# Kernel tuning notes

Measured on AMD Instinct MI355X. Metric: run time of the kernel, lower is better.

## Reference

```python
import jax, jax.numpy as jnp
import numpy as np

N = 50000        # n_nodes
E = 640000       # n_edges
D = 128          # d_model (in_dim == out_dim)
H = 8            # num_heads
DH = D // H      # head dim = 16
EPS = 1e-5


def _batchnorm(x, g, b):
    # BatchNorm1d, training-mode batch statistics (biased variance)
    mu = jnp.mean(x, axis=0)
    var = jnp.mean((x - mu) ** 2, axis=0)
    return (x - mu) * jax.lax.rsqrt(var + EPS) * g + b


def setup_inputs() -> dict:
    key = jax.random.key(0)
    ks = jax.random.split(key, 16)
    s = 0.05
    h = jax.random.normal(ks[0], (N, D), jnp.float32)
    src = jax.random.randint(ks[1], (E,), 0, N)
    # guarantee every node has >= 1 incoming edge (avoids z == 0)
    dst = jnp.concatenate([jnp.arange(N), jax.random.randint(ks[2], (E - N,), 0, N)])
    return {
        "h": h,
        "src": src,
        "dst": dst,
        "WQ": jax.random.normal(ks[3], (D, D), jnp.float32) * s,
        "WK": jax.random.normal(ks[4], (D, D), jnp.float32) * s,
        "WV": jax.random.normal(ks[5], (D, D), jnp.float32) * s,
        "WO": jax.random.normal(ks[6], (D, D), jnp.float32) * s,
        "bO": jnp.zeros((D,), jnp.float32),
        "W1": jax.random.normal(ks[7], (2 * D, D), jnp.float32) * s,
        "b1": jnp.zeros((2 * D,), jnp.float32),
        "W2": jax.random.normal(ks[8], (D, 2 * D), jnp.float32) * s,
        "b2": jnp.zeros((D,), jnp.float32),
        "bn1_g": jnp.ones((D,), jnp.float32),
        "bn1_b": jnp.zeros((D,), jnp.float32),
        "bn2_g": jnp.ones((D,), jnp.float32),
        "bn2_b": jnp.zeros((D,), jnp.float32),
    }


def reference(h, src, dst, WQ, WK, WV, WO, bO, W1, b1, W2, b2, bn1_g, bn1_b, bn2_g, bn2_b):
    n = h.shape[0]
    # projections -> [N, H, DH]
    Q = (h @ WQ.T).reshape(n, H, DH)
    K = (h @ WK.T).reshape(n, H, DH)
    V = (h @ WV.T).reshape(n, H, DH)
    # per-edge score: sum(K[src] * Q[dst]) -> [E, H]; clamp/exp (scaled_exp)
    score = jnp.sum(K[src] * Q[dst], axis=-1) / np.sqrt(DH)
    score = jnp.exp(jnp.clip(score, -5.0, 5.0))
    # scatter-sum weighted values and normalizers to destination nodes
    wV = jax.ops.segment_sum(V[src] * score[..., None], dst, num_segments=n)  # [N,H,DH]
    z = jax.ops.segment_sum(score, dst, num_segments=n)                       # [N,H]
    attn = (wV / z[..., None]).reshape(n, D)
    # O projection + residual + BN1
    h1 = _batchnorm(h + (attn @ WO.T + bO), bn1_g, bn1_b)
    # FFN + residual + BN2
    f = jax.nn.relu(h1 @ W1.T + b1) @ W2.T + b2
    return _batchnorm(h1 + f, bn2_g, bn2_b)
```

## Files before the change

### kernel.cpp

```cpp
#include <hip/hip_runtime.h>
#include <math.h>


#define ND128 16384
typedef _Float16 f16;
typedef __attribute__((ext_vector_type(8))) _Float16 h8;
typedef __attribute__((ext_vector_type(4))) _Float16 h4;
typedef __attribute__((ext_vector_type(2))) _Float16 h2;
typedef __attribute__((ext_vector_type(4))) float f4;

__device__ __forceinline__ float fdot2h(h2 a, h2 b) {
#if __has_builtin(__builtin_amdgcn_fdot2)
    return __builtin_amdgcn_fdot2(a, b, 0.f, false);
#else
    return (float)a[0] * (float)b[0] + (float)a[1] * (float)b[1];
#endif
}

__device__ __forceinline__ float fast_exp2(float x) {
#if __has_builtin(__builtin_amdgcn_exp2f)
    return __builtin_amdgcn_exp2f(x);
#else
    return exp2f(x);
#endif
}

template <int CTRL>
__device__ __forceinline__ float dppadd(float x) {
    int t = __builtin_amdgcn_update_dpp(0, __float_as_int(x), CTRL, 0xF, 0xF, false);
    return x + __int_as_float(t);
}
__device__ __forceinline__ float wsum8(float p) {
    p = dppadd<0xB1>(p);
    p = dppadd<0x4E>(p);
    p = dppadd<0x141>(p);
    return p;
}

__global__ __launch_bounds__(256) void k_prep(
    const float* __restrict__ h, f16* __restrict__ hb,
    const float* __restrict__ WQ, const float* __restrict__ WK,
    const float* __restrict__ WV, const float* __restrict__ WO,
    const float* __restrict__ W2,
    f16* __restrict__ Wqb, f16* __restrict__ Wkb,
    f16* __restrict__ Wvb, f16* __restrict__ Wob, f16* __restrict__ W2b,
    float* __restrict__ bn, int* __restrict__ cursor, int N)
{
    const int slab = blockIdx.x, my = blockIdx.y;
    const int tid = threadIdx.x;
    if (my == 0) {
        if (tid < 128) {
            int ci = slab * 128 + tid;
            if (ci < N) cursor[ci] = 0;
        }
        if (slab == 6) { bn[tid] = 0.f; bn[tid + 256] = 0.f; }
    }
#pragma unroll
    for (int it2 = 0; it2 < 4; ++it2) {
        int it = my * 4 + it2;
        int cid = it * 256 + tid;
        int lane = cid & 63;
        int m = (cid >> 6) & 7;
        int kb = cid >> 9;
        int row = slab * 128 + m * 16 + (lane & 15);
        int col = kb * 32 + (lane >> 4) * 8;
        f16 o8[8];
        if (row < N) {
            const float* p = h + (size_t)row * 128 + col;
            float4 f0 = *(const float4*)p;
            float4 f1 = *(const float4*)(p + 4);
            o8[0] = (f16)f0.x; o8[1] = (f16)f0.y; o8[2] = (f16)f0.z; o8[3] = (f16)f0.w;
            o8[4] = (f16)f1.x; o8[5] = (f16)f1.y; o8[6] = (f16)f1.z; o8[7] = (f16)f1.w;
        } else {
#pragma unroll
            for (int j = 0; j < 8; ++j) o8[j] = (f16)0.f;
        }
        *(h8*)(hb + (size_t)slab * ND128 + (size_t)cid * 8) = *(const h8*)o8;
    }
    if (slab < 6 && my == 1) {
        const float* Wsrc; f16* dst; int K, base;
        if (slab < 4) {
            Wsrc = slab == 0 ? WQ : slab == 1 ? WK : slab == 2 ? WV : WO;
            dst  = slab == 0 ? Wqb : slab == 1 ? Wkb : slab == 2 ? Wvb : Wob;
            K = 128; base = 0;
        } else {
            Wsrc = W2; dst = W2b; K = 256; base = (slab - 4) * 2048;
        }
#pragma unroll
        for (int it = 0; it < 8; ++it) {
            int cid = base + it * 256 + tid;
            int lane = cid & 63;
            int kb, nt;
            if (K == 128) { kb = (cid >> 6) & 3; nt = cid >> 8; }
            else          { kb = (cid >> 6) & 7; nt = cid >> 9; }
            int row = nt * 16 + (lane & 15);
            int col = kb * 32 + (lane >> 4) * 8;
            const float* p = Wsrc + (size_t)row * K + col;
            f16 o8[8];
#pragma unroll
            for (int j = 0; j < 8; ++j) o8[j] = (f16)p[j];
            *(h8*)(dst + (size_t)cid * 8) = *(const h8*)o8;
        }
    }
}

__global__ __launch_bounds__(256) void k_qkv(
    const f16* __restrict__ hb, const f16* __restrict__ Wqb,
    const f16* __restrict__ Wkb, const f16* __restrict__ Wvb,
    f16* __restrict__ Qb, f16* __restrict__ Kh,
    f16* __restrict__ Vh, int N)
{
    const int slab = blockIdx.x, oidx = blockIdx.y, mh = blockIdx.z;
    const int w = threadIdx.x >> 6, lane = threadIdx.x & 63;
    const f16* __restrict__ Wb = oidx == 0 ? Wqb : oidx == 1 ? Wkb : Wvb;
    f16* __restrict__ Ob = oidx == 0 ? Qb : oidx == 1 ? Kh : Vh;
    const f16* A = hb + (size_t)slab * ND128;

    h8 bfr[2][4];
#pragma unroll
    for (int nt = 0; nt < 2; ++nt)
#pragma unroll
        for (int kb = 0; kb < 4; ++kb)
            bfr[nt][kb] = *(const h8*)(Wb + (size_t)(((2 * w + nt) * 4 + kb) * 64 + lane) * 8);

    f4 acc[4][2];
    f4 zero = {0.f, 0.f, 0.f, 0.f};
#pragma unroll
    for (int m = 0; m < 4; ++m) { acc[m][0] = zero; acc[m][1] = zero; }

#pragma unroll
    for (int m = 0; m < 4; ++m) {
        int mg = mh * 4 + m;
#pragma unroll
        for (int kb = 0; kb < 4; ++kb) {
            h8 a = *(const h8*)(A + (size_t)((kb * 8 + mg) * 64 + lane) * 8);
            acc[m][0] = __builtin_amdgcn_mfma_f32_16x16x32_f16(bfr[0][kb], a, acc[m][0], 0, 0, 0);
            acc[m][1] = __builtin_amdgcn_mfma_f32_16x16x32_f16(bfr[1][kb], a, acc[m][1], 0, 0, 0);
        }
    }

    const int rl = lane & 15, quad = lane >> 4;
#pragma unroll
    for (int m = 0; m < 4; ++m) {
        int gr = slab * 128 + (mh * 4 + m) * 16 + rl;
        if (gr < N) {
#pragma unroll
            for (int nt = 0; nt < 2; ++nt) {
                h4 o;
                o[0] = (f16)acc[m][nt][0]; o[1] = (f16)acc[m][nt][1];
                o[2] = (f16)acc[m][nt][2]; o[3] = (f16)acc[m][nt][3];
                *(h4*)(Ob + (size_t)gr * 128 + w * 32 + nt * 16 + quad * 4) = o;
            }
        }
    }
}

__global__ __launch_bounds__(256) void k_hist(
    const int* __restrict__ dst, int* __restrict__ cursor, int E)
{
    int e = blockIdx.x * 256 + threadIdx.x;
    if (e < E) atomicAdd(&cursor[dst[e]], 1);
}

__global__ __launch_bounds__(256) void k_scanA(
    const int* __restrict__ cnt, int* __restrict__ bsum, int N)
{
    const int t = threadIdx.x;
    int base = blockIdx.x * 2048 + t * 8;
    int s = 0;
#pragma unroll
    for (int j = 0; j < 8; ++j) {
        int idx = base + j;
        if (idx < N) s += cnt[idx];
    }
#pragma unroll
    for (int off = 32; off; off >>= 1) s += __shfl_down(s, off, 64);
    __shared__ int ws4[4];
    if ((t & 63) == 0) ws4[t >> 6] = s;
    __syncthreads();
    if (t == 0) bsum[blockIdx.x] = ws4[0] + ws4[1] + ws4[2] + ws4[3];
}

__global__ __launch_bounds__(256) void k_scanC(
    const int* __restrict__ cnt, const int* __restrict__ bsum,
    int* __restrict__ rowptr, int* __restrict__ cursor, int N, int nsb)
{
    const int t = threadIdx.x, b = blockIdx.x;
    __shared__ int sboff;
    if (t == 0) {
        int r = 0;
        for (int i2 = 0; i2 < b; ++i2) r += bsum[i2];
        sboff = r;
    }
    if (t == 64 && b == nsb - 1) {
        int r = 0;
        for (int i2 = 0; i2 < nsb; ++i2) r += bsum[i2];
        rowptr[N] = r;
    }
    int base = b * 2048 + t * 8;
    int loc[8];
    int s = 0;
#pragma unroll
    for (int j = 0; j < 8; ++j) {
        int idx = base + j;
        loc[j] = (idx < N) ? cnt[idx] : 0;
        s += loc[j];
    }
    __shared__ int part[256];
    part[t] = s;
    __syncthreads();
    for (int off = 1; off < 256; off <<= 1) {
        int v = (t >= off) ? part[t - off] : 0;
        __syncthreads();
        part[t] += v;
        __syncthreads();
    }
    int run = sboff + (t ? part[t - 1] : 0);
#pragma unroll
    for (int j = 0; j < 8; ++j) {
        int idx = base + j;
        if (idx < N) { rowptr[idx] = run; cursor[idx] = run; run += loc[j]; }
    }
}

__global__ __launch_bounds__(256) void k_scatter(
    const int* __restrict__ src, const int* __restrict__ dst,
    int* __restrict__ cursor, int* __restrict__ csr_src, int E)
{
    int e = blockIdx.x * 256 + threadIdx.x;
    if (e < E) {
        int pos = atomicAdd(&cursor[dst[e]], 1);
        csr_src[pos] = src[e];
    }
}

__global__ __launch_bounds__(256) void k_attn(
    const f16* __restrict__ Qb, const f16* __restrict__ Kh,
    const f16* __restrict__ Vh,
    const int* __restrict__ rowptr, const int* __restrict__ csr_src,
    f16* __restrict__ attnf, int N)
{
    const int node = blockIdx.x * 4 + (threadIdx.x >> 6);
    const int lane = threadIdx.x & 63;
    if (node >= N) return;
    const int beg = rowptr[node], end = rowptr[node + 1];

    h2 qs;
    {
        h2 q2 = ((const h2*)(Qb + (size_t)node * 128))[lane];
        const float SCL = 0.25f * 1.44269504f;
        qs[0] = (f16)((float)q2[0] * SCL);
        qs[1] = (f16)((float)q2[1] * SCL);
    }
    const float CLP = 5.f * 1.44269504f;

    const h2* __restrict__ K2 = (const h2*)Kh;
    const h2* __restrict__ V2 = (const h2*)Vh;

    h2 accA, accB;
    accA[0] = (f16)0.f; accA[1] = (f16)0.f;
    accB[0] = (f16)0.f; accB[1] = (f16)0.f;
    float z = 0.f;

    int i = beg;
    for (; i + 3 < end; i += 4) {
        int s0 = csr_src[i], s1 = csr_src[i + 1];
        int s2 = csr_src[i + 2], s3 = csr_src[i + 3];
        h2 k0 = K2[(size_t)s0 * 64 + lane];
        h2 k1 = K2[(size_t)s1 * 64 + lane];
        h2 k2 = K2[(size_t)s2 * 64 + lane];
        h2 k3 = K2[(size_t)s3 * 64 + lane];
        h2 v0 = V2[(size_t)s0 * 64 + lane];
        h2 v1 = V2[(size_t)s1 * 64 + lane];
        h2 v2 = V2[(size_t)s2 * 64 + lane];
        h2 v3 = V2[(size_t)s3 * 64 + lane];
        float p0 = fdot2h(qs, k0);
        float p1 = fdot2h(qs, k1);
        float p2 = fdot2h(qs, k2);
        float p3 = fdot2h(qs, k3);
        p0 = wsum8(p0); p1 = wsum8(p1); p2 = wsum8(p2); p3 = wsum8(p3);
        float sc0 = fast_exp2(fminf(fmaxf(p0, -CLP), CLP));
        float sc1 = fast_exp2(fminf(fmaxf(p1, -CLP), CLP));
        float sc2 = fast_exp2(fminf(fmaxf(p2, -CLP), CLP));
        float sc3 = fast_exp2(fminf(fmaxf(p3, -CLP), CLP));
        z += sc0 + sc1 + sc2 + sc3;
        h2 c0; c0[0] = (f16)sc0; c0[1] = (f16)sc0;
        h2 c1; c1[0] = (f16)sc1; c1[1] = (f16)sc1;
        h2 c2; c2[0] = (f16)sc2; c2[1] = (f16)sc2;
        h2 c3; c3[0] = (f16)sc3; c3[1] = (f16)sc3;
        accA += c0 * v0; accB += c1 * v1;
        accA += c2 * v2; accB += c3 * v3;
    }
    for (; i < end; ++i) {
        int s0 = csr_src[i];
        h2 k0 = K2[(size_t)s0 * 64 + lane];
        h2 v0 = V2[(size_t)s0 * 64 + lane];
        float p0 = fdot2h(qs, k0);
        p0 = wsum8(p0);
        float sc0 = fast_exp2(fminf(fmaxf(p0, -CLP), CLP));
        z += sc0;
        h2 c0; c0[0] = (f16)sc0; c0[1] = (f16)sc0;
        accA += c0 * v0;
    }

    float inv = 1.f / z;
    float ax = ((float)accA[0] + (float)accB[0]) * inv;
    float ay = ((float)accA[1] + (float)accB[1]) * inv;
    h2 o2;
    o2[0] = (f16)ax; o2[1] = (f16)ay;
    int slab = node >> 7, m = (node >> 4) & 7, lr = node & 15;
    int kb = lane >> 4, quad2 = (lane & 15) >> 2, j = (lane & 3) * 2;
    *(h2*)(attnf + (size_t)slab * ND128 +
           (size_t)(((kb * 8 + m) * 64 + lr + 16 * quad2) * 8 + j)) = o2;
}

__global__ __launch_bounds__(256) void k_oproj(
    const f16* __restrict__ attnf, const f16* __restrict__ Wob,
    const float* __restrict__ h, const float* __restrict__ bO,
    f16* __restrict__ t1b, float* __restrict__ bn, int N)
{
    __shared__ float csum[128], csq[128];
    const int tid = threadIdx.x, slab = blockIdx.x, mh = blockIdx.y;
    const int w = tid >> 6, lane = tid & 63;
    if (tid < 128) { csum[tid] = 0.f; csq[tid] = 0.f; }
    __syncthreads();
    const f16* A = attnf + (size_t)slab * ND128;

    h8 bfr[2][4];
#pragma unroll
    for (int nt = 0; nt < 2; ++nt)
#pragma unroll
        for (int kb = 0; kb < 4; ++kb)
            bfr[nt][kb] = *(const h8*)(Wob + (size_t)(((2 * w + nt) * 4 + kb) * 64 + lane) * 8);

    f4 acc[4][2];
    f4 zero = {0.f, 0.f, 0.f, 0.f};
#pragma unroll
    for (int m = 0; m < 4; ++m) { acc[m][0] = zero; acc[m][1] = zero; }
#pragma unroll
    for (int m = 0; m < 4; ++m) {
        int mg = mh * 4 + m;
#pragma unroll
        for (int kb = 0; kb < 4; ++kb) {
            h8 a = *(const h8*)(A + (size_t)((kb * 8 + mg) * 64 + lane) * 8);
            acc[m][0] = __builtin_amdgcn_mfma_f32_16x16x32_f16(bfr[0][kb], a, acc[m][0], 0, 0, 0);
            acc[m][1] = __builtin_amdgcn_mfma_f32_16x16x32_f16(bfr[1][kb], a, acc[m][1], 0, 0, 0);
        }
    }

    const int rl = lane & 15, quad = lane >> 4;
    float4 bo[2];
#pragma unroll
    for (int nt = 0; nt < 2; ++nt)
        bo[nt] = *(const float4*)(bO + w * 32 + nt * 16 + quad * 4);
    float pcs[2][4], pcq[2][4];
#pragma unroll
    for (int nt = 0; nt < 2; ++nt)
#pragma unroll
        for (int r = 0; r < 4; ++r) { pcs[nt][r] = 0.f; pcq[nt][r] = 0.f; }

#pragma unroll
    for (int m = 0; m < 4; ++m) {
        int mg = mh * 4 + m;
        int gr = slab * 128 + mg * 16 + rl;
        if (gr < N) {
#pragma unroll
            for (int nt = 0; nt < 2; ++nt) {
                int col0 = w * 32 + nt * 16 + quad * 4;
                float4 hv = *(const float4*)(h + (size_t)gr * 128 + col0);
                float v0 = acc[m][nt][0] + hv.x + bo[nt].x;
                float v1 = acc[m][nt][1] + hv.y + bo[nt].y;
                float v2 = acc[m][nt][2] + hv.z + bo[nt].z;
                float v3 = acc[m][nt][3] + hv.w + bo[nt].w;
                h4 o; o[0] = (f16)v0; o[1] = (f16)v1; o[2] = (f16)v2; o[3] = (f16)v3;
                *(h4*)(t1b + (size_t)slab * ND128 +
                       (size_t)(((w * 8 + mg) * 64 + (nt * 2 + (quad >> 1)) * 16 + rl) * 8 +
                                (quad & 1) * 4)) = o;
                pcs[nt][0] += v0; pcq[nt][0] += v0 * v0;
                pcs[nt][1] += v1; pcq[nt][1] += v1 * v1;
                pcs[nt][2] += v2; pcq[nt][2] += v2 * v2;
                pcs[nt][3] += v3; pcq[nt][3] += v3 * v3;
            }
        }
    }
#pragma unroll
    for (int nt = 0; nt < 2; ++nt)
#pragma unroll
        for (int r = 0; r < 4; ++r) {
            float s = pcs[nt][r], q = pcq[nt][r];
            s += __shfl_xor(s, 8, 16); q += __shfl_xor(q, 8, 16);
            s += __shfl_xor(s, 4, 16); q += __shfl_xor(q, 4, 16);
            s += __shfl_xor(s, 2, 16); q += __shfl_xor(q, 2, 16);
            s += __shfl_xor(s, 1, 16); q += __shfl_xor(q, 1, 16);
            if (rl == 0) {
                int cl = w * 32 + nt * 16 + quad * 4 + r;
                atomicAdd(&csum[cl], s);
                atomicAdd(&csq[cl], q);
            }
        }
    __syncthreads();
    if (tid < 128) {
        atomicAdd(bn + tid, csum[tid]);
        atomicAdd(bn + 128 + tid, csq[tid]);
    }
}

__global__ __launch_bounds__(128) void k_fold1(
    const float* __restrict__ bn, const float* __restrict__ g1,
    const float* __restrict__ bb1, const float* __restrict__ W1,
    const float* __restrict__ b1, f16* __restrict__ W1b,
    float* __restrict__ badj, float* __restrict__ sfold,
    float* __restrict__ bfold, int N)
{
    const int o = blockIdx.x, i = threadIdx.x;
    float invN = 1.f / (float)N;
    float mu = bn[i] * invN;
    float var = bn[128 + i] * invN - mu * mu;
    float s = g1[i] * rsqrtf(var + 1e-5f);
    float bb = bb1[i] - mu * s;
    if (o == 0) { sfold[i] = s; bfold[i] = bb; }
    float wv = W1[(size_t)o * 128 + i];
    __shared__ float red[128];
    red[i] = wv * bb;
    const int nt = o >> 4, lanelow = o & 15;
    const int kb = i >> 5, quad = (i >> 3) & 3, j = i & 7;
    W1b[(size_t)(((nt * 4 + kb) * 64 + lanelow + 16 * quad) * 8 + j)] = (f16)(wv * s);
    __syncthreads();
#pragma unroll
    for (int off = 64; off; off >>= 1) {
        if (i < off) red[i] += red[i + off];
        __syncthreads();
    }
    if (i == 0) badj[o] = b1[o] + red[0];
}

__global__ __launch_bounds__(256) void k_ffn1(
    const f16* __restrict__ t1b, const f16* __restrict__ W1b,
    const float* __restrict__ badj, f16* __restrict__ ub, int N)
{
    const int slab = blockIdx.x, ch = blockIdx.y, mh = blockIdx.z;
    const int w = threadIdx.x >> 6, lane = threadIdx.x & 63;
    const f16* A = t1b + (size_t)slab * ND128;

    h8 bfr[2][4];
#pragma unroll
    for (int nt = 0; nt < 2; ++nt)
#pragma unroll
        for (int kb = 0; kb < 4; ++kb) {
            int ntg = ch * 8 + 2 * w + nt;
            bfr[nt][kb] = *(const h8*)(W1b + (size_t)((ntg * 4 + kb) * 64 + lane) * 8);
        }

    f4 acc[4][2];
    f4 zero = {0.f, 0.f, 0.f, 0.f};
#pragma unroll
    for (int m = 0; m < 4; ++m) { acc[m][0] = zero; acc[m][1] = zero; }
#pragma unroll
    for (int m = 0; m < 4; ++m) {
        int mg = mh * 4 + m;
#pragma unroll
        for (int kb = 0; kb < 4; ++kb) {
            h8 a = *(const h8*)(A + (size_t)((kb * 8 + mg) * 64 + lane) * 8);
            acc[m][0] = __builtin_amdgcn_mfma_f32_16x16x32_f16(bfr[0][kb], a, acc[m][0], 0, 0, 0);
            acc[m][1] = __builtin_amdgcn_mfma_f32_16x16x32_f16(bfr[1][kb], a, acc[m][1], 0, 0, 0);
        }
    }

    const int rl = lane & 15, quad = lane >> 4;
    const int kbu = ch * 4 + w;
    float4 ba[2];
#pragma unroll
    for (int nt = 0; nt < 2; ++nt)
        ba[nt] = *(const float4*)(badj + ch * 128 + w * 32 + nt * 16 + quad * 4);
#pragma unroll
    for (int m = 0; m < 4; ++m) {
        int mg = mh * 4 + m;
        int gr = slab * 128 + mg * 16 + rl;
        if (gr < N) {
#pragma unroll
            for (int nt = 0; nt < 2; ++nt) {
                h4 o;
                o[0] = (f16)fmaxf(acc[m][nt][0] + ba[nt].x, 0.f);
                o[1] = (f16)fmaxf(acc[m][nt][1] + ba[nt].y, 0.f);
                o[2] = (f16)fmaxf(acc[m][nt][2] + ba[nt].z, 0.f);
                o[3] = (f16)fmaxf(acc[m][nt][3] + ba[nt].w, 0.f);
                *(h4*)(ub + (size_t)slab * 32768 +
                       (size_t)(((kbu * 8 + mg) * 64 + (nt * 2 + (quad >> 1)) * 16 + rl) * 8 +
                                (quad & 1) * 4)) = o;
            }
        }
    }
}

__global__ __launch_bounds__(256) void k_ffn2(
    const f16* __restrict__ ub, const f16* __restrict__ W2b,
    const f16* __restrict__ t1b,
    const float* __restrict__ sfold, const float* __restrict__ bfold,
    const float* __restrict__ b2, float* __restrict__ out,
    float* __restrict__ bn, int N)
{
    __shared__ float csum[128], csq[128], sS[128], sB[128];
    const int tid = threadIdx.x, slab = blockIdx.x, mh = blockIdx.y;
    const int w = tid >> 6, lane = tid & 63;
    if (tid < 128) {
        csum[tid] = 0.f; csq[tid] = 0.f;
        sS[tid] = sfold[tid]; sB[tid] = bfold[tid] + b2[tid];
    }
    __syncthreads();
    const f16* A = ub + (size_t)slab * 32768;
    const f16* T1 = t1b + (size_t)slab * ND128;

    h8 bfr[2][8];
#pragma unroll
    for (int nt = 0; nt < 2; ++nt)
#pragma unroll
        for (int kb = 0; kb < 8; ++kb)
            bfr[nt][kb] = *(const h8*)(W2b + (size_t)(((2 * w + nt) * 8 + kb) * 64 + lane) * 8);

    f4 acc[4][2];
    f4 zero = {0.f, 0.f, 0.f, 0.f};
#pragma unroll
    for (int m = 0; m < 4; ++m) { acc[m][0] = zero; acc[m][1] = zero; }
#pragma unroll
    for (int m = 0; m < 4; ++m) {
        int mg = mh * 4 + m;
#pragma unroll
        for (int kb = 0; kb < 8; ++kb) {
            h8 a = *(const h8*)(A + (size_t)((kb * 8 + mg) * 64 + lane) * 8);
            acc[m][0] = __builtin_amdgcn_mfma_f32_16x16x32_f16(bfr[0][kb], a, acc[m][0], 0, 0, 0);
            acc[m][1] = __builtin_amdgcn_mfma_f32_16x16x32_f16(bfr[1][kb], a, acc[m][1], 0, 0, 0);
        }
    }

    const int rl = lane & 15, quad = lane >> 4;
    float pcs[2][4], pcq[2][4];
#pragma unroll
    for (int nt = 0; nt < 2; ++nt)
#pragma unroll
        for (int r = 0; r < 4; ++r) { pcs[nt][r] = 0.f; pcq[nt][r] = 0.f; }

#pragma unroll
    for (int m = 0; m < 4; ++m) {
        int mg = mh * 4 + m;
        int gr = slab * 128 + mg * 16 + rl;
        if (gr < N) {
#pragma unroll
            for (int nt = 0; nt < 2; ++nt) {
                int col0 = w * 32 + nt * 16 + quad * 4;
                h4 t1v = *(const h4*)(T1 +
                    (size_t)(((w * 8 + mg) * 64 + (nt * 2 + (quad >> 1)) * 16 + rl) * 8 +
                             (quad & 1) * 4));
                float4 ss = *(const float4*)&sS[col0];
                float4 sb = *(const float4*)&sB[col0];
                float4 o;
                o.x = acc[m][nt][0] + fmaf(ss.x, (float)t1v[0], sb.x);
                o.y = acc[m][nt][1] + fmaf(ss.y, (float)t1v[1], sb.y);
                o.z = acc[m][nt][2] + fmaf(ss.z, (float)t1v[2], sb.z);
                o.w = acc[m][nt][3] + fmaf(ss.w, (float)t1v[3], sb.w);
                *(float4*)(out + (size_t)gr * 128 + col0) = o;
                pcs[nt][0] += o.x; pcq[nt][0] += o.x * o.x;
                pcs[nt][1] += o.y; pcq[nt][1] += o.y * o.y;
                pcs[nt][2] += o.z; pcq[nt][2] += o.z * o.z;
                pcs[nt][3] += o.w; pcq[nt][3] += o.w * o.w;
            }
        }
    }
#pragma unroll
    for (int nt = 0; nt < 2; ++nt)
#pragma unroll
        for (int r = 0; r < 4; ++r) {
            float s = pcs[nt][r], q = pcq[nt][r];
            s += __shfl_xor(s, 8, 16); q += __shfl_xor(q, 8, 16);
            s += __shfl_xor(s, 4, 16); q += __shfl_xor(q, 4, 16);
            s += __shfl_xor(s, 2, 16); q += __shfl_xor(q, 2, 16);
            s += __shfl_xor(s, 1, 16); q += __shfl_xor(q, 1, 16);
            if (rl == 0) {
                int cl = w * 32 + nt * 16 + quad * 4 + r;
                atomicAdd(&csum[cl], s);
                atomicAdd(&csq[cl], q);
            }
        }
    __syncthreads();
    if (tid < 128) {
        atomicAdd(bn + 256 + tid, csum[tid]);
        atomicAdd(bn + 384 + tid, csq[tid]);
    }
}

__global__ __launch_bounds__(256) void k_bn2(
    float* __restrict__ out, const float* __restrict__ bn,
    const float* __restrict__ g2, const float* __restrict__ bb2, int N)
{
    __shared__ float sS[128], sB[128];
    const int tid = threadIdx.x;
    if (tid < 128) {
        float invN = 1.f / (float)N;
        float mu = bn[256 + tid] * invN;
        float var = bn[384 + tid] * invN - mu * mu;
        float scl = g2[tid] * rsqrtf(var + 1e-5f);
        sS[tid] = scl;
        sB[tid] = bb2[tid] - mu * scl;
    }
    __syncthreads();
    size_t idx = (size_t)blockIdx.x * 256 + tid;
    size_t total = (size_t)N * 32;
    if (idx < total) {
        int c0 = (int)((idx * 4) & 127);
        float4 v = *(const float4*)(out + idx * 4);
        v.x = fmaf(v.x, sS[c0 + 0], sB[c0 + 0]);
        v.y = fmaf(v.y, sS[c0 + 1], sB[c0 + 1]);
        v.z = fmaf(v.z, sS[c0 + 2], sB[c0 + 2]);
        v.w = fmaf(v.w, sS[c0 + 3], sB[c0 + 3]);
        *(float4*)(out + idx * 4) = v;
    }
}

extern "C" void kernel_launch(void* const* d_in, const int* in_sizes, int n_in,
                              void* d_out, int out_size, void* d_ws, size_t ws_size,
                              hipStream_t stream)
{
    const float* h   = (const float*)d_in[0];
    const int*   src = (const int*)d_in[1];
    const int*   dst = (const int*)d_in[2];
    const float* WQ  = (const float*)d_in[3];
    const float* WK  = (const float*)d_in[4];
    const float* WV  = (const float*)d_in[5];
    const float* WO  = (const float*)d_in[6];
    const float* bO  = (const float*)d_in[7];
    const float* W1  = (const float*)d_in[8];
    const float* b1  = (const float*)d_in[9];
    const float* W2  = (const float*)d_in[10];
    const float* b2  = (const float*)d_in[11];
    const float* g1  = (const float*)d_in[12];
    const float* bb1 = (const float*)d_in[13];
    const float* g2  = (const float*)d_in[14];
    const float* bb2 = (const float*)d_in[15];
    float* out = (float*)d_out;

    int N = in_sizes[0] / 128;
    int E = in_sizes[1];
    const int slabs = (N + 127) / 128;
    const int nsb = (N + 2047) / 2048;
    const size_t B1 = (size_t)slabs * 32768;

    char* Wp = (char*)d_ws;
    f16* hb  = (f16*)Wp;
    f16* Qb  = (f16*)(Wp + B1);
    f16* Kh  = (f16*)(Wp + 2 * B1);
    f16* Vh  = (f16*)(Wp + 3 * B1);
    f16* ub  = (f16*)(Wp + B1);
    f16* t1b = (f16*)(Wp + 3 * B1);
    const size_t base = 4 * B1;
    f16* Wqb = (f16*)(Wp + base);
    f16* Wkb = (f16*)(Wp + base + 32768);
    f16* Wvb = (f16*)(Wp + base + 65536);
    f16* Wob = (f16*)(Wp + base + 98304);
    f16* W1b = (f16*)(Wp + base + 131072);
    f16* W2b = (f16*)(Wp + base + 196608);
    float* badj  = (float*)(Wp + base + 262144);
    float* sfold = (float*)(Wp + base + 263168);
    float* bfold = (float*)(Wp + base + 263680);
    float* bn    = (float*)(Wp + base + 264192);
    int* cursor  = (int*)(Wp + base + 266240);
    int* rowptr  = (int*)(Wp + base + 266240 + (size_t)N * 4);
    int* csr     = (int*)(Wp + base + 266240 + (size_t)N * 8 + 8);
    int* bsum    = (int*)((char*)csr + (size_t)E * 4);

    k_prep<<<dim3(slabs, 2), 256, 0, stream>>>(h, hb, WQ, WK, WV, WO, W2,
                                               Wqb, Wkb, Wvb, Wob, W2b, bn, cursor, N);
    k_qkv<<<dim3(slabs, 3, 2), 256, 0, stream>>>(hb, Wqb, Wkb, Wvb, Qb, Kh, Vh, N);
    k_hist<<<(E + 255) / 256, 256, 0, stream>>>(dst, cursor, E);
    k_scanA<<<nsb, 256, 0, stream>>>(cursor, bsum, N);
    k_scanC<<<nsb, 256, 0, stream>>>(cursor, bsum, rowptr, cursor, N, nsb);
    k_scatter<<<(E + 255) / 256, 256, 0, stream>>>(src, dst, cursor, csr, E);
    k_attn<<<(N + 3) / 4, 256, 0, stream>>>(Qb, Kh, Vh, rowptr, csr, hb, N);
    k_oproj<<<dim3(slabs, 2), 256, 0, stream>>>(hb, Wob, h, bO, t1b, bn, N);
    k_fold1<<<256, 128, 0, stream>>>(bn, g1, bb1, W1, b1, W1b, badj, sfold, bfold, N);
    k_ffn1<<<dim3(slabs, 2, 2), 256, 0, stream>>>(t1b, W1b, badj, ub, N);
    k_ffn2<<<dim3(slabs, 2), 256, 0, stream>>>(ub, W2b, t1b, sfold, bfold, b2, out, bn, N);
    k_bn2<<<(int)(((size_t)N * 32 + 255) / 256), 256, 0, stream>>>(out, bn, g2, bb2, N);
}
```

Measured before the change: 329.0 us.

## Fuse histogram into prep, fold scan into QKV kernel, interleave K/V rows

The edge histogram now runs as extra blocks of the prep kernel, after a memset of the cursor and BN buffers. The two-pass scan becomes a single-pass decoupled scan whose blocks chain through ready flags, and it is launched as extra blocks of the QKV projection kernel. K and V are written interleaved per node so each gathered source row serves both loads, and the attention gather loop is unrolled to 8 edges for more loads in flight. The aim is fewer launches and better gather locality; in exchange, the scan blocks spin-wait on their predecessors, which relies on earlier blocks being scheduled first.

Result: slower. 340.1 us (+3.4%).

```diff
diff --git a/kernel.cpp b/kernel.cpp
--- a/kernel.cpp
+++ b/kernel.cpp
@@ -37,24 +37,24 @@
     return p;
 }
 
-__global__ __launch_bounds__(256) void k_prep(
+__global__ __launch_bounds__(256) void k_prep_hist(
     const float* __restrict__ h, f16* __restrict__ hb,
     const float* __restrict__ WQ, const float* __restrict__ WK,
     const float* __restrict__ WV, const float* __restrict__ WO,
     const float* __restrict__ W2,
     f16* __restrict__ Wqb, f16* __restrict__ Wkb,
     f16* __restrict__ Wvb, f16* __restrict__ Wob, f16* __restrict__ W2b,
-    float* __restrict__ bn, int* __restrict__ cursor, int N)
-{
-    const int slab = blockIdx.x, my = blockIdx.y;
+    int* __restrict__ cursor, const int* __restrict__ dst,
+    int N, int E, int nhb)
+{
     const int tid = threadIdx.x;
-    if (my == 0) {
-        if (tid < 128) {
-            int ci = slab * 128 + tid;
-            if (ci < N) cursor[ci] = 0;
-        }
-        if (slab == 6) { bn[tid] = 0.f; bn[tid + 256] = 0.f; }
-    }
+    if (blockIdx.x < (unsigned)nhb) {
+        int e = blockIdx.x * 256 + tid;
+        if (e < E) atomicAdd(&cursor[dst[e]], 1);
+        return;
+    }
+    const int p = blockIdx.x - nhb;
+    const int slab = p >> 1, my = p & 1;
 #pragma unroll
     for (int it2 = 0; it2 < 4; ++it2) {
         int it = my * 4 + it2;
@@ -66,9 +66,9 @@
         int col = kb * 32 + (lane >> 4) * 8;
         f16 o8[8];
         if (row < N) {
-            const float* p = h + (size_t)row * 128 + col;
-            float4 f0 = *(const float4*)p;
-            float4 f1 = *(const float4*)(p + 4);
+            const float* pp = h + (size_t)row * 128 + col;
+            float4 f0 = *(const float4*)pp;
+            float4 f1 = *(const float4*)(pp + 4);
             o8[0] = (f16)f0.x; o8[1] = (f16)f0.y; o8[2] = (f16)f0.z; o8[3] = (f16)f0.w;
             o8[4] = (f16)f1.x; o8[5] = (f16)f1.y; o8[6] = (f16)f1.z; o8[7] = (f16)f1.w;
         } else {
@@ -78,13 +78,13 @@
         *(h8*)(hb + (size_t)slab * ND128 + (size_t)cid * 8) = *(const h8*)o8;
     }
     if (slab < 6 && my == 1) {
-        const float* Wsrc; f16* dst; int K, base;
+        const float* Wsrc; f16* dstw; int K, base;
         if (slab < 4) {
             Wsrc = slab == 0 ? WQ : slab == 1 ? WK : slab == 2 ? WV : WO;
-            dst  = slab == 0 ? Wqb : slab == 1 ? Wkb : slab == 2 ? Wvb : Wob;
+            dstw = slab == 0 ? Wqb : slab == 1 ? Wkb : slab == 2 ? Wvb : Wob;
             K = 128; base = 0;
         } else {
-            Wsrc = W2; dst = W2b; K = 256; base = (slab - 4) * 2048;
+            Wsrc = W2; dstw = W2b; K = 256; base = (slab - 4) * 2048;
         }
 #pragma unroll
         for (int it = 0; it < 8; ++it) {
@@ -95,25 +95,72 @@
             else          { kb = (cid >> 6) & 7; nt = cid >> 9; }
             int row = nt * 16 + (lane & 15);
             int col = kb * 32 + (lane >> 4) * 8;
-            const float* p = Wsrc + (size_t)row * K + col;
+            const float* pp = Wsrc + (size_t)row * K + col;
             f16 o8[8];
 #pragma unroll
-            for (int j = 0; j < 8; ++j) o8[j] = (f16)p[j];
-            *(h8*)(dst + (size_t)cid * 8) = *(const h8*)o8;
-        }
-    }
-}
-
-__global__ __launch_bounds__(256) void k_qkv(
+            for (int j = 0; j < 8; ++j) o8[j] = (f16)pp[j];
+            *(h8*)(dstw + (size_t)cid * 8) = *(const h8*)o8;
+        }
+    }
+}
+
+__global__ __launch_bounds__(256) void k_qkv_scan(
     const f16* __restrict__ hb, const f16* __restrict__ Wqb,
     const f16* __restrict__ Wkb, const f16* __restrict__ Wvb,
-    f16* __restrict__ Qb, f16* __restrict__ Kh,
-    f16* __restrict__ Vh, int N)
-{
-    const int slab = blockIdx.x, oidx = blockIdx.y, mh = blockIdx.z;
-    const int w = threadIdx.x >> 6, lane = threadIdx.x & 63;
+    f16* __restrict__ Qb, f16* __restrict__ KVb,
+    int* __restrict__ cursor, int* __restrict__ rowptr,
+    int* __restrict__ ready, int N, int nsb)
+{
+    const int tid = threadIdx.x;
+    if (blockIdx.x < (unsigned)nsb) {
+        const int b = blockIdx.x;
+        int base = b * 2048 + tid * 8;
+        int loc[8];
+        int s = 0;
+#pragma unroll
+        for (int j = 0; j < 8; ++j) {
+            int idx = base + j;
+            loc[j] = (idx < N) ? cursor[idx] : 0;
+            s += loc[j];
+        }
+        __shared__ int part[256];
+        part[tid] = s;
+        __syncthreads();
+        for (int off = 1; off < 256; off <<= 1) {
+            int v = (tid >= off) ? part[tid - off] : 0;
+            __syncthreads();
+            part[tid] += v;
+            __syncthreads();
+        }
+        __shared__ int sboff_sh;
+        if (tid == 0) {
+            int prev = 0;
+            if (b > 0) {
+                int r;
+                while ((r = __hip_atomic_load(&ready[b - 1], __ATOMIC_ACQUIRE,
+                                              __HIP_MEMORY_SCOPE_AGENT)) == 0) {}
+                prev = r - 1;
+            }
+            int btotal = part[255];
+            __hip_atomic_store(&ready[b], prev + btotal + 1, __ATOMIC_RELEASE,
+                               __HIP_MEMORY_SCOPE_AGENT);
+            sboff_sh = prev;
+            if (b == nsb - 1) rowptr[N] = prev + btotal;
+        }
+        __syncthreads();
+        int run = sboff_sh + (tid ? part[tid - 1] : 0);
+#pragma unroll
+        for (int j = 0; j < 8; ++j) {
+            int idx = base + j;
+            if (idx < N) { rowptr[idx] = run; cursor[idx] = run; run += loc[j]; }
+        }
+        return;
+    }
+    const int b2 = blockIdx.x - nsb;
+    const int slab = b2 / 6, r6 = b2 % 6;
+    const int oidx = r6 >> 1, mh = r6 & 1;
+    const int w = tid >> 6, lane = tid & 63;
     const f16* __restrict__ Wb = oidx == 0 ? Wqb : oidx == 1 ? Wkb : Wvb;
-    f16* __restrict__ Ob = oidx == 0 ? Qb : oidx == 1 ? Kh : Vh;
     const f16* A = hb + (size_t)slab * ND128;
 
     h8 bfr[2][4];
@@ -149,77 +196,14 @@
                 h4 o;
                 o[0] = (f16)acc[m][nt][0]; o[1] = (f16)acc[m][nt][1];
                 o[2] = (f16)acc[m][nt][2]; o[3] = (f16)acc[m][nt][3];
-                *(h4*)(Ob + (size_t)gr * 128 + w * 32 + nt * 16 + quad * 4) = o;
+                int col = w * 32 + nt * 16 + quad * 4;
+                if (oidx == 0) {
+                    *(h4*)(Qb + (size_t)gr * 128 + col) = o;
+                } else {
+                    *(h4*)(KVb + (size_t)gr * 256 + (oidx == 1 ? col : 128 + col)) = o;
+                }
             }
         }
-    }
-}
-
-__global__ __launch_bounds__(256) void k_hist(
-    const int* __restrict__ dst, int* __restrict__ cursor, int E)
-{
-    int e = blockIdx.x * 256 + threadIdx.x;
-    if (e < E) atomicAdd(&cursor[dst[e]], 1);
-}
-
-__global__ __launch_bounds__(256) void k_scanA(
-    const int* __restrict__ cnt, int* __restrict__ bsum, int N)
-{
-    const int t = threadIdx.x;
-    int base = blockIdx.x * 2048 + t * 8;
-    int s = 0;
-#pragma unroll
-    for (int j = 0; j < 8; ++j) {
-        int idx = base + j;
-        if (idx < N) s += cnt[idx];
-    }
-#pragma unroll
-    for (int off = 32; off; off >>= 1) s += __shfl_down(s, off, 64);
-    __shared__ int ws4[4];
-    if ((t & 63) == 0) ws4[t >> 6] = s;
-    __syncthreads();
-    if (t == 0) bsum[blockIdx.x] = ws4[0] + ws4[1] + ws4[2] + ws4[3];
-}
-
-__global__ __launch_bounds__(256) void k_scanC(
-    const int* __restrict__ cnt, const int* __restrict__ bsum,
-    int* __restrict__ rowptr, int* __restrict__ cursor, int N, int nsb)
-{
-    const int t = threadIdx.x, b = blockIdx.x;
-    __shared__ int sboff;
-    if (t == 0) {
-        int r = 0;
-        for (int i2 = 0; i2 < b; ++i2) r += bsum[i2];
-        sboff = r;
-    }
-    if (t == 64 && b == nsb - 1) {
-        int r = 0;
-        for (int i2 = 0; i2 < nsb; ++i2) r += bsum[i2];
-        rowptr[N] = r;
-    }
-    int base = b * 2048 + t * 8;
-    int loc[8];
-    int s = 0;
-#pragma unroll
-    for (int j = 0; j < 8; ++j) {
-        int idx = base + j;
-        loc[j] = (idx < N) ? cnt[idx] : 0;
-        s += loc[j];
-    }
-    __shared__ int part[256];
-    part[t] = s;
-    __syncthreads();
-    for (int off = 1; off < 256; off <<= 1) {
-        int v = (t >= off) ? part[t - off] : 0;
-        __syncthreads();
-        part[t] += v;
-        __syncthreads();
-    }
-    int run = sboff + (t ? part[t - 1] : 0);
-#pragma unroll
-    for (int j = 0; j < 8; ++j) {
-        int idx = base + j;
-        if (idx < N) { rowptr[idx] = run; cursor[idx] = run; run += loc[j]; }
     }
 }
 
@@ -235,8 +219,7 @@
 }
 
 __global__ __launch_bounds__(256) void k_attn(
-    const f16* __restrict__ Qb, const f16* __restrict__ Kh,
-    const f16* __restrict__ Vh,
+    const f16* __restrict__ Qb, const f16* __restrict__ KVb,
     const int* __restrict__ rowptr, const int* __restrict__ csr_src,
     f16* __restrict__ attnf, int N)
 {
@@ -254,8 +237,7 @@
     }
     const float CLP = 5.f * 1.44269504f;
 
-    const h2* __restrict__ K2 = (const h2*)Kh;
-    const h2* __restrict__ V2 = (const h2*)Vh;
+    const h2* __restrict__ KV2 = (const h2*)KVb;
 
     h2 accA, accB;
     accA[0] = (f16)0.f; accA[1] = (f16)0.f;
@@ -263,40 +245,58 @@
     float z = 0.f;
 
     int i = beg;
-    for (; i + 3 < end; i += 4) {
-        int s0 = csr_src[i], s1 = csr_src[i + 1];
-        int s2 = csr_src[i + 2], s3 = csr_src[i + 3];
-        h2 k0 = K2[(size_t)s0 * 64 + lane];
-        h2 k1 = K2[(size_t)s1 * 64 + lane];
-        h2 k2 = K2[(size_t)s2 * 64 + lane];
-        h2 k3 = K2[(size_t)s3 * 64 + lane];
-        h2 v0 = V2[(size_t)s0 * 64 + lane];
-        h2 v1 = V2[(size_t)s1 * 64 + lane];
-        h2 v2 = V2[(size_t)s2 * 64 + lane];
-        h2 v3 = V2[(size_t)s3 * 64 + lane];
-        float p0 = fdot2h(qs, k0);
-        float p1 = fdot2h(qs, k1);
-        float p2 = fdot2h(qs, k2);
-        float p3 = fdot2h(qs, k3);
-        p0 = wsum8(p0); p1 = wsum8(p1); p2 = wsum8(p2); p3 = wsum8(p3);
-        float sc0 = fast_exp2(fminf(fmaxf(p0, -CLP), CLP));
-        float sc1 = fast_exp2(fminf(fmaxf(p1, -CLP), CLP));
-        float sc2 = fast_exp2(fminf(fmaxf(p2, -CLP), CLP));
-        float sc3 = fast_exp2(fminf(fmaxf(p3, -CLP), CLP));
-        z += sc0 + sc1 + sc2 + sc3;
-        h2 c0; c0[0] = (f16)sc0; c0[1] = (f16)sc0;
-        h2 c1; c1[0] = (f16)sc1; c1[1] = (f16)sc1;
-        h2 c2; c2[0] = (f16)sc2; c2[1] = (f16)sc2;
-        h2 c3; c3[0] = (f16)sc3; c3[1] = (f16)sc3;
-        accA += c0 * v0; accB += c1 * v1;
-        accA += c2 * v2; accB += c3 * v3;
+    for (; i + 7 < end; i += 8) {
+        int s[8];
+#pragma unroll
+        for (int u = 0; u < 8; ++u) s[u] = csr_src[i + u];
+        h2 kk[8], vv[8];
+#pragma unroll
+        for (int u = 0; u < 8; ++u) {
+            const h2* row = KV2 + (size_t)s[u] * 128;
+            kk[u] = row[lane];
+            vv[u] = row[64 + lane];
+        }
+        float sc[8];
+#pragma unroll
+        for (int u = 0; u < 8; ++u) {
+            float p = wsum8(fdot2h(qs, kk[u]));
+            sc[u] = fast_exp2(fminf(fmaxf(p, -CLP), CLP));
+        }
+#pragma unroll
+        for (int u = 0; u < 8; ++u) z += sc[u];
+#pragma unroll
+        for (int u = 0; u < 8; ++u) {
+            h2 c; c[0] = (f16)sc[u]; c[1] = (f16)sc[u];
+            if (u & 1) accB += c * vv[u]; else accA += c * vv[u];
+        }
+    }
+    if (i + 3 < end) {
+        int s[4];
+#pragma unroll
+        for (int u = 0; u < 4; ++u) s[u] = csr_src[i + u];
+        h2 kk[4], vv[4];
+#pragma unroll
+        for (int u = 0; u < 4; ++u) {
+            const h2* row = KV2 + (size_t)s[u] * 128;
+            kk[u] = row[lane];
+            vv[u] = row[64 + lane];
+        }
+#pragma unroll
+        for (int u = 0; u < 4; ++u) {
+            float p = wsum8(fdot2h(qs, kk[u]));
+            float scu = fast_exp2(fminf(fmaxf(p, -CLP), CLP));
+            z += scu;
+            h2 c; c[0] = (f16)scu; c[1] = (f16)scu;
+            if (u & 1) accB += c * vv[u]; else accA += c * vv[u];
+        }
+        i += 4;
     }
     for (; i < end; ++i) {
         int s0 = csr_src[i];
-        h2 k0 = K2[(size_t)s0 * 64 + lane];
-        h2 v0 = V2[(size_t)s0 * 64 + lane];
-        float p0 = fdot2h(qs, k0);
-        p0 = wsum8(p0);
+        const h2* row = KV2 + (size_t)s0 * 128;
+        h2 k0 = row[lane];
+        h2 v0 = row[64 + lane];
+        float p0 = wsum8(fdot2h(qs, k0));
         float sc0 = fast_exp2(fminf(fmaxf(p0, -CLP), CLP));
         z += sc0;
         h2 c0; c0[0] = (f16)sc0; c0[1] = (f16)sc0;
@@ -641,13 +641,13 @@
     int E = in_sizes[1];
     const int slabs = (N + 127) / 128;
     const int nsb = (N + 2047) / 2048;
+    const int nhb = (E + 255) / 256;
     const size_t B1 = (size_t)slabs * 32768;
 
     char* Wp = (char*)d_ws;
     f16* hb  = (f16*)Wp;
     f16* Qb  = (f16*)(Wp + B1);
-    f16* Kh  = (f16*)(Wp + 2 * B1);
-    f16* Vh  = (f16*)(Wp + 3 * B1);
+    f16* KVb = (f16*)(Wp + 2 * B1);
     f16* ub  = (f16*)(Wp + B1);
     f16* t1b = (f16*)(Wp + 3 * B1);
     const size_t base = 4 * B1;
@@ -661,19 +661,18 @@
     float* sfold = (float*)(Wp + base + 263168);
     float* bfold = (float*)(Wp + base + 263680);
     float* bn    = (float*)(Wp + base + 264192);
-    int* cursor  = (int*)(Wp + base + 266240);
-    int* rowptr  = (int*)(Wp + base + 266240 + (size_t)N * 4);
-    int* csr     = (int*)(Wp + base + 266240 + (size_t)N * 8 + 8);
-    int* bsum    = (int*)((char*)csr + (size_t)E * 4);
-
-    k_prep<<<dim3(slabs, 2), 256, 0, stream>>>(h, hb, WQ, WK, WV, WO, W2,
-                                               Wqb, Wkb, Wvb, Wob, W2b, bn, cursor, N);
-    k_qkv<<<dim3(slabs, 3, 2), 256, 0, stream>>>(hb, Wqb, Wkb, Wvb, Qb, Kh, Vh, N);
-    k_hist<<<(E + 255) / 256, 256, 0, stream>>>(dst, cursor, E);
-    k_scanA<<<nsb, 256, 0, stream>>>(cursor, bsum, N);
-    k_scanC<<<nsb, 256, 0, stream>>>(cursor, bsum, rowptr, cursor, N, nsb);
-    k_scatter<<<(E + 255) / 256, 256, 0, stream>>>(src, dst, cursor, csr, E);
-    k_attn<<<(N + 3) / 4, 256, 0, stream>>>(Qb, Kh, Vh, rowptr, csr, hb, N);
+    int* ready   = (int*)(Wp + base + 266240);
+    int* cursor  = (int*)(Wp + base + 266496);
+    int* rowptr  = (int*)(Wp + base + 266496 + (size_t)N * 4);
+    int* csr     = (int*)(Wp + base + 266496 + (size_t)N * 8 + 8);
+
+    hipMemsetAsync(Wp + base + 264192, 0, 2304 + (size_t)N * 4, stream);
+    k_prep_hist<<<nhb + slabs * 2, 256, 0, stream>>>(
+        h, hb, WQ, WK, WV, WO, W2, Wqb, Wkb, Wvb, Wob, W2b, cursor, dst, N, E, nhb);
+    k_qkv_scan<<<nsb + slabs * 6, 256, 0, stream>>>(
+        hb, Wqb, Wkb, Wvb, Qb, KVb, cursor, rowptr, ready, N, nsb);
+    k_scatter<<<nhb, 256, 0, stream>>>(src, dst, cursor, csr, E);
+    k_attn<<<(N + 3) / 4, 256, 0, stream>>>(Qb, KVb, rowptr, csr, hb, N);
     k_oproj<<<dim3(slabs, 2), 256, 0, stream>>>(hb, Wob, h, bO, t1b, bn, N);
     k_fold1<<<256, 128, 0, stream>>>(bn, g1, bb1, W1, b1, W1b, badj, sfold, bfold, N);
     k_ffn1<<<dim3(slabs, 2, 2), 256, 0, stream>>>(t1b, W1b, badj, ub, N);
```
